# Optimization experiments

Hardware: AMD Instinct MI355X
Metric: run time of the kernel (lower is better)

## Reference

```python
import jax, jax.numpy as jnp
import numpy as np

SR = 24000          # sampling_rate
MAX_H = 60          # min(n_harmonics=100, 60)


def _interp_linear(x, T):
    """Linear upsample along axis 1, align_corners=True. x: [B, C, F] -> [B, T, F]."""
    B, C, F = x.shape
    src = jnp.arange(T, dtype=x.dtype) * ((C - 1) / (T - 1))
    i0 = jnp.clip(jnp.floor(src).astype(jnp.int32), 0, C - 2)
    frac = (src - i0.astype(x.dtype))[None, :, None]
    return x[:, i0, :] * (1.0 - frac) + x[:, i0 + 1, :] * frac


def setup_inputs() -> dict:
    key = jax.random.key(0)
    k1, k2, k3, k4, k5 = jax.random.split(key, 5)
    B, T, H, C, NF = 8, 48000, MAX_H, 100, 5
    f0 = 100.0 + 300.0 * jax.random.uniform(k1, (B, T, 1), dtype=jnp.float32)
    amplitudes = jax.random.uniform(k2, (B, T, H), dtype=jnp.float32)
    formant_freqs = 200.0 + 3300.0 * jax.random.uniform(k3, (B, C, NF), dtype=jnp.float32)
    formant_bws = 50.0 + 150.0 * jax.random.uniform(k4, (B, C, NF), dtype=jnp.float32)
    formant_amps = jax.random.uniform(k5, (B, C, NF), dtype=jnp.float32)
    initial_phase = jnp.zeros((B, 1, 1), dtype=jnp.float32)
    return {"f0": f0, "amplitudes": amplitudes, "formant_freqs": formant_freqs,
            "formant_bws": formant_bws, "formant_amps": formant_amps,
            "initial_phase": initial_phase}


def reference(f0, amplitudes, formant_freqs, formant_bws, formant_amps, initial_phase):
    B, T, _ = f0.shape
    f0 = jax.lax.stop_gradient(f0)                    # torch: f0.detach()
    voiced = (f0[..., 0] > 0).astype(f0.dtype)        # [B, T]
    phase = jnp.cumsum(2.0 * np.pi * f0 / SR, axis=1) + initial_phase  # [B, T, 1]

    ff = _interp_linear(formant_freqs, T)             # [B, T, NF]
    fb = _interp_linear(formant_bws, T)
    fa = _interp_linear(formant_amps, T)

    h = jnp.arange(1, MAX_H + 1, dtype=f0.dtype)      # [H]
    h_freq = f0 * h                                   # [B, T, H]
    nyq = (h_freq < SR / 2).astype(f0.dtype)          # [B, T, H]

    # formant resonance factor: prod over formants of (1 + amp*bw^2/((h_freq-freq)^2+bw^2))
    factor = jnp.ones_like(h_freq)
    for f in range(ff.shape[-1]):                     # NF = 5, small fixed loop
        freq = ff[:, :, f:f + 1]
        bw = fb[:, :, f:f + 1]
        amp = fa[:, :, f:f + 1]
        factor = factor * (1.0 + amp * bw * bw / ((h_freq - freq) ** 2 + bw * bw))

    osc = jnp.sin(phase * h)                          # [B, T, H]
    signal = jnp.sum(osc * amplitudes * factor * nyq, axis=-1) * voiced  # [B, T]

    final_phase = jax.lax.stop_gradient(phase[:, -1:, :] % (2.0 * np.pi))  # [B, 1, 1]
    return signal, final_phase
```

## Files before the change

### kernel.cpp

```cpp
#include <hip/hip_runtime.h>
#include <math.h>

#define SRATE   24000.0
#define NB      8
#define NT      48000
#define NH      60
#define NC      100
#define NFMT    5
#define CTS     64
#define NCH     (NT / CTS)
#define NPAIR   (NCH / 2)
#define TWO_PI  6.283185307179586476925286766559
#define PSC     (1.0f / 1024.0f)
#define NYQS    11.71875f

typedef float v2f __attribute__((ext_vector_type(2)));

__global__ __launch_bounds__(256) void k_partial(const float* __restrict__ f0,
                                                 double* __restrict__ part) {
    int b = blockIdx.y;
    int ch = blockIdx.x * 4 + (threadIdx.x >> 6);
    int lane = threadIdx.x & 63;
    if (ch < NCH) {
        int t = ch * CTS + lane;
        double q = (double)f0[b * NT + t];
        #pragma unroll
        for (int off = 32; off > 0; off >>= 1)
            q += __shfl_down(q, off, 64);
        if (lane == 0) part[b * NCH + ch] = q;
    }
}

__global__ __launch_bounds__(256) void k_main(const float* __restrict__ f0,
                                              const float* __restrict__ amps,
                                              const float* __restrict__ ffq,
                                              const float* __restrict__ fbw,
                                              const float* __restrict__ fam,
                                              const float* __restrict__ initp,
                                              const double* __restrict__ part,
                                              float* __restrict__ out) {
    int b = blockIdx.y;
    int cp = blockIdx.x * 4 + (threadIdx.x >> 6);
    int lane = threadIdx.x & 63;
    if (cp >= NPAIR) return;
    int ch0 = cp * 2;
    int t0 = cp * 128;
    int g0 = lane >> 2, j = lane & 3;

    const float* ab = amps + (size_t)b * NT * NH;

    const float4* r0 = (const float4*)(ab + (size_t)(t0 + g0) * NH);
    float4 A0 = r0[j * 4], A1 = r0[j * 4 + 1], A2 = r0[j * 4 + 2];
    float4 A3 = (j < 3) ? r0[j * 4 + 3] : make_float4(0.f, 0.f, 0.f, 0.f);
    const float4* r1 = (const float4*)(ab + (size_t)(t0 + 16 + g0) * NH);
    float4 B0 = r1[j * 4], B1 = r1[j * 4 + 1], B2 = r1[j * 4 + 2];
    float4 B3 = (j < 3) ? r1[j * 4 + 3] : make_float4(0.f, 0.f, 0.f, 0.f);

    const double* pb = part + b * NCH;
    double sl = 0.0;
    #pragma unroll
    for (int k = 0; k < 12; ++k) {
        int idx = k * 64 + lane;
        double v = (idx < NCH) ? pb[idx] : 0.0;
        if (idx < ch0) sl += v;
    }
    #pragma unroll
    for (int off = 1; off < 64; off <<= 1)
        sl += __shfl_xor(sl, off, 64);

    double initrev = (double)initp[b] * (1.0 / TWO_PI);

    if (cp == 0) {
        double sa = 0.0;
        #pragma unroll
        for (int k = 0; k < 12; ++k) {
            int idx = k * 64 + lane;
            if (idx < NCH) sa += pb[idx];
        }
        #pragma unroll
        for (int off = 1; off < 64; off <<= 1)
            sa += __shfl_xor(sa, off, 64);
        if (lane == 0) {
            double rv = sa * (1.0 / SRATE) + initrev;
            out[NB * NT + b] = (float)((rv - floor(rv)) * TWO_PI);
        }
    }

    float revA, f0sA, revB, f0sB;
    float fqA[NFMT], c1A[NFMT], c2A[NFMT], fqB[NFMT], c1B[NFMT], c2B[NFMT];

    auto chunk_pre = [&](int tl, double prefd, float& rev_o, float& f0s_o,
                         float (&fqo)[NFMT], float (&c1o)[NFMT],
                         float (&c2o)[NFMT]) -> double {
        float f0v = f0[b * NT + tl];
        double inc = (double)f0v;
        #pragma unroll
        for (int off = 1; off < 64; off <<= 1) {
            double n = __shfl_up(inc, off, 64);
            if (lane >= off) inc += n;
        }
        double rev = (prefd + inc) * (1.0 / SRATE) + initrev;
        rev_o = (float)(rev - floor(rev));
        f0s_o = f0v * PSC;
        double srcd = (double)tl * (99.0 / 47999.0);
        int i0 = (int)srcd;
        if (i0 > NC - 2) i0 = NC - 2;
        float frac = (float)(srcd - (double)i0);
        float omf = 1.0f - frac;
        const float* Fq = ffq + (b * NC + i0) * NFMT;
        const float* Bw = fbw + (b * NC + i0) * NFMT;
        const float* Am = fam + (b * NC + i0) * NFMT;
        #pragma unroll
        for (int f = 0; f < NFMT; ++f) {
            float fqv = Fq[f] * omf + Fq[NFMT + f] * frac;
            float bwv = Bw[f] * omf + Bw[NFMT + f] * frac;
            float amv = Am[f] * omf + Am[NFMT + f] * frac;
            float bws = bwv * PSC;
            fqo[f] = fqv * PSC;
            c2o[f] = bws * bws;
            c1o[f] = amv * c2o[f];
        }
        return __shfl(inc, 63, 64);
    };

    double tot0 = chunk_pre(t0 + lane, sl, revA, f0sA, fqA, c1A, c2A);
    chunk_pre(t0 + 64 + lane, sl + tot0, revB, f0sB, fqB, c1B, c2B);

    auto do_pass = [&](int p, float revLane, float f0sLane,
                       const float (&fqL)[NFMT], const float (&c1L)[NFMT],
                       const float (&c2L)[NFMT],
                       float4 q0, float4 q1, float4 q2, float4 q3) {
        int gp = ((p & 3) << 4) + g0;
        float f0s   = __shfl(f0sLane, gp, 64);
        float rev_g = __shfl(revLane, gp, 64);
        float fq[NFMT], c1[NFMT], c2[NFMT];
        #pragma unroll
        for (int f = 0; f < NFMT; ++f) {
            fq[f] = __shfl(fqL[f], gp, 64);
            c1[f] = __shfl(c1L[f], gp, 64);
            c2[f] = __shfl(c2L[f], gp, 64);
        }
        float hb = (float)(j << 4);
        auto sd = [&](float k) {
            return __builtin_amdgcn_sinf(
                __builtin_amdgcn_fractf((hb + k) * rev_g));
        };
        float cc = __builtin_amdgcn_cosf(
            __builtin_amdgcn_fractf(2.0f * rev_g));
        v2f cv = {2.0f * cc, 2.0f * cc};
        v2f pr0 = {sd(1.0f), sd(2.0f)};
        v2f pr1 = {sd(3.0f), sd(4.0f)};
        v2f pr2 = cv * pr1 - pr0;
        v2f pr3 = cv * pr2 - pr1;
        v2f pr4 = {sd(9.0f), sd(10.0f)};
        v2f pr5 = {sd(11.0f), sd(12.0f)};
        v2f pr6 = cv * pr5 - pr4;
        v2f pr7 = cv * pr6 - pr5;
        v2f acc2 = {0.0f, 0.0f};
        auto pairf = [&](float h1, v2f sn, float a0, float a1) {
            v2f hfl = {h1, h1 + 1.0f};
            v2f hs = f0s * hfl;
            v2f pN = {1.0f, 1.0f}, pD = {1.0f, 1.0f};
            #pragma unroll
            for (int f = 0; f < NFMT; ++f) {
                v2f d = hs - fq[f];
                v2f e = d * d + c2[f];
                pN *= e + c1[f];
                pD *= e;
            }
            float R = __builtin_amdgcn_rcpf(pD.x * pD.y);
            v2f fac = {pN.x * pD.y * R, pN.y * pD.x * R};
            v2f fm;
            fm.x = (hs.x < NYQS) ? fac.x : 0.0f;
            fm.y = (hs.y < NYQS) ? fac.y : 0.0f;
            v2f aa = {a0, a1};
            acc2 += (sn * aa) * fm;
        };
        pairf(hb + 1.0f,  pr0, q0.x, q0.y);
        pairf(hb + 3.0f,  pr1, q0.z, q0.w);
        pairf(hb + 5.0f,  pr2, q1.x, q1.y);
        pairf(hb + 7.0f,  pr3, q1.z, q1.w);
        pairf(hb + 9.0f,  pr4, q2.x, q2.y);
        pairf(hb + 11.0f, pr5, q2.z, q2.w);
        pairf(hb + 13.0f, pr6, q3.x, q3.y);
        pairf(hb + 15.0f, pr7, q3.z, q3.w);
        float acc = acc2.x + acc2.y;
        acc += __shfl_xor(acc, 1, 64);
        acc += __shfl_xor(acc, 2, 64);
        if (j == 0) {
            if (!(f0s > 0.0f)) acc = 0.0f;
            out[b * NT + t0 + (p << 4) + g0] = acc;
        }
    };

    #pragma unroll 1
    for (int pg = 0; pg < 8; pg += 2) {
        bool cB = pg >= 4;
        float revL = cB ? revB : revA;
        float f0sL = cB ? f0sB : f0sA;
        float fqL[NFMT], c1L[NFMT], c2L[NFMT];
        #pragma unroll
        for (int f = 0; f < NFMT; ++f) {
            fqL[f] = cB ? fqB[f] : fqA[f];
            c1L[f] = cB ? c1B[f] : c1A[f];
            c2L[f] = cB ? c2B[f] : c2A[f];
        }
        do_pass(pg, revL, f0sL, fqL, c1L, c2L, A0, A1, A2, A3);
        if (pg < 6) {
            const float4* rr =
                (const float4*)(ab + (size_t)(t0 + (pg + 2) * 16 + g0) * NH);
            A0 = rr[j * 4]; A1 = rr[j * 4 + 1]; A2 = rr[j * 4 + 2];
            A3 = (j < 3) ? rr[j * 4 + 3] : make_float4(0.f, 0.f, 0.f, 0.f);
        }
        do_pass(pg + 1, revL, f0sL, fqL, c1L, c2L, B0, B1, B2, B3);
        if (pg < 6) {
            const float4* rr =
                (const float4*)(ab + (size_t)(t0 + (pg + 3) * 16 + g0) * NH);
            B0 = rr[j * 4]; B1 = rr[j * 4 + 1]; B2 = rr[j * 4 + 2];
            B3 = (j < 3) ? rr[j * 4 + 3] : make_float4(0.f, 0.f, 0.f, 0.f);
        }
    }
}

extern "C" void kernel_launch(void* const* d_in, const int* in_sizes, int n_in,
                              void* d_out, int out_size, void* d_ws, size_t ws_size,
                              hipStream_t stream) {
    const float* f0    = (const float*)d_in[0];
    const float* amps  = (const float*)d_in[1];
    const float* ffq   = (const float*)d_in[2];
    const float* fbw   = (const float*)d_in[3];
    const float* fam   = (const float*)d_in[4];
    const float* initp = (const float*)d_in[5];
    float* out = (float*)d_out;

    double* part = (double*)d_ws;

    dim3 gpart((NCH + 3) / 4, NB);
    k_partial<<<gpart, 256, 0, stream>>>(f0, part);
    dim3 gmain((NPAIR + 3) / 4, NB);
    k_main<<<gmain, 256, 0, stream>>>(f0, amps, ffq, fbw, fam, initp, part, out);
}
```

Measured before the change: 33.20 us.

## Hoist all global loads up front and triple-buffer amplitude rows across passes

Issues the f0, formant table, and partial-sum loads at kernel start. Triple-buffers the amplitude rows (three passes in flight instead of two) and fully unrolls the eight passes. The two prefix scans are merged into a single interleaved shuffle loop, and the total-sum reduction runs in every wave instead of only the first. The goal is to hide global memory latency behind the sine/formant math. The costs are more registers (launch bounds now ask for 3 blocks per SM) and some redundant reduction work.

```diff
diff --git a/kernel.cpp b/kernel.cpp
--- a/kernel.cpp
+++ b/kernel.cpp
@@ -31,14 +31,14 @@
     }
 }
 
-__global__ __launch_bounds__(256) void k_main(const float* __restrict__ f0,
-                                              const float* __restrict__ amps,
-                                              const float* __restrict__ ffq,
-                                              const float* __restrict__ fbw,
-                                              const float* __restrict__ fam,
-                                              const float* __restrict__ initp,
-                                              const double* __restrict__ part,
-                                              float* __restrict__ out) {
+__global__ __launch_bounds__(256, 3) void k_main(const float* __restrict__ f0,
+                                                 const float* __restrict__ amps,
+                                                 const float* __restrict__ ffq,
+                                                 const float* __restrict__ fbw,
+                                                 const float* __restrict__ fam,
+                                                 const float* __restrict__ initp,
+                                                 const double* __restrict__ part,
+                                                 float* __restrict__ out) {
     int b = blockIdx.y;
     int cp = blockIdx.x * 4 + (threadIdx.x >> 6);
     int lane = threadIdx.x & 63;
@@ -46,85 +46,100 @@
     int ch0 = cp * 2;
     int t0 = cp * 128;
     int g0 = lane >> 2, j = lane & 3;
-
+    const float4 f4z = make_float4(0.f, 0.f, 0.f, 0.f);
     const float* ab = amps + (size_t)b * NT * NH;
 
-    const float4* r0 = (const float4*)(ab + (size_t)(t0 + g0) * NH);
-    float4 A0 = r0[j * 4], A1 = r0[j * 4 + 1], A2 = r0[j * 4 + 2];
-    float4 A3 = (j < 3) ? r0[j * 4 + 3] : make_float4(0.f, 0.f, 0.f, 0.f);
-    const float4* r1 = (const float4*)(ab + (size_t)(t0 + 16 + g0) * NH);
-    float4 B0 = r1[j * 4], B1 = r1[j * 4 + 1], B2 = r1[j * 4 + 2];
-    float4 B3 = (j < 3) ? r1[j * 4 + 3] : make_float4(0.f, 0.f, 0.f, 0.f);
-
+    float f0A = f0[b * NT + t0 + lane];
+    float f0B = f0[b * NT + t0 + 64 + lane];
+
+    double srcA = (double)(t0 + lane) * (99.0 / 47999.0);
+    int iA = (int)srcA; if (iA > NC - 2) iA = NC - 2;
+    float frA = (float)(srcA - (double)iA), omA = 1.0f - frA;
+    double srcB = (double)(t0 + 64 + lane) * (99.0 / 47999.0);
+    int iB = (int)srcB; if (iB > NC - 2) iB = NC - 2;
+    float frB = (float)(srcB - (double)iB), omB = 1.0f - frB;
+
+    const float* FqA = ffq + (b * NC + iA) * NFMT;
+    const float* BwA = fbw + (b * NC + iA) * NFMT;
+    const float* AmA = fam + (b * NC + iA) * NFMT;
+    const float* FqB = ffq + (b * NC + iB) * NFMT;
+    const float* BwB = fbw + (b * NC + iB) * NFMT;
+    const float* AmB = fam + (b * NC + iB) * NFMT;
+    float tA[30], tB[30];
+    #pragma unroll
+    for (int f = 0; f < NFMT; ++f) {
+        tA[f]      = FqA[f]; tA[5 + f]  = FqA[NFMT + f];
+        tA[10 + f] = BwA[f]; tA[15 + f] = BwA[NFMT + f];
+        tA[20 + f] = AmA[f]; tA[25 + f] = AmA[NFMT + f];
+        tB[f]      = FqB[f]; tB[5 + f]  = FqB[NFMT + f];
+        tB[10 + f] = BwB[f]; tB[15 + f] = BwB[NFMT + f];
+        tB[20 + f] = AmB[f]; tB[25 + f] = AmB[NFMT + f];
+    }
     const double* pb = part + b * NCH;
-    double sl = 0.0;
+    double pv[12];
     #pragma unroll
     for (int k = 0; k < 12; ++k) {
         int idx = k * 64 + lane;
-        double v = (idx < NCH) ? pb[idx] : 0.0;
-        if (idx < ch0) sl += v;
-    }
-    #pragma unroll
-    for (int off = 1; off < 64; off <<= 1)
+        pv[k] = (idx < NCH) ? pb[idx] : 0.0;
+    }
+
+    #define AMPLD(S0, S1, S2, S3, p)                                          \
+        { const float4* rr =                                                  \
+              (const float4*)(ab + (size_t)(t0 + (p) * 16 + g0) * NH);        \
+          S0 = rr[j * 4]; S1 = rr[j * 4 + 1]; S2 = rr[j * 4 + 2];             \
+          S3 = (j < 3) ? rr[j * 4 + 3] : f4z; }
+    float4 P0, P1, P2, P3, Q0, Q1, Q2, Q3, R0, R1, R2, R3;
+    AMPLD(P0, P1, P2, P3, 0)
+    AMPLD(Q0, Q1, Q2, Q3, 1)
+    AMPLD(R0, R1, R2, R3, 2)
+
+    double sl = 0.0, sa = 0.0;
+    #pragma unroll
+    for (int k = 0; k < 12; ++k) {
+        int idx = k * 64 + lane;
+        sa += pv[k];
+        if (idx < ch0) sl += pv[k];
+    }
+    #pragma unroll
+    for (int off = 1; off < 64; off <<= 1) {
         sl += __shfl_xor(sl, off, 64);
-
+        sa += __shfl_xor(sa, off, 64);
+    }
     double initrev = (double)initp[b] * (1.0 / TWO_PI);
-
-    if (cp == 0) {
-        double sa = 0.0;
-        #pragma unroll
-        for (int k = 0; k < 12; ++k) {
-            int idx = k * 64 + lane;
-            if (idx < NCH) sa += pb[idx];
-        }
-        #pragma unroll
-        for (int off = 1; off < 64; off <<= 1)
-            sa += __shfl_xor(sa, off, 64);
-        if (lane == 0) {
-            double rv = sa * (1.0 / SRATE) + initrev;
-            out[NB * NT + b] = (float)((rv - floor(rv)) * TWO_PI);
-        }
-    }
-
-    float revA, f0sA, revB, f0sB;
+    if (cp == 0 && lane == 0) {
+        double rv = sa * (1.0 / SRATE) + initrev;
+        out[NB * NT + b] = (float)((rv - floor(rv)) * TWO_PI);
+    }
+
+    double incA = (double)f0A, incB = (double)f0B;
+    #pragma unroll
+    for (int off = 1; off < 64; off <<= 1) {
+        double nA = __shfl_up(incA, off, 64);
+        double nB = __shfl_up(incB, off, 64);
+        if (lane >= off) { incA += nA; incB += nB; }
+    }
+    double totA = __shfl(incA, 63, 64);
+    double rA = (sl + incA) * (1.0 / SRATE) + initrev;
+    double rB = (sl + totA + incB) * (1.0 / SRATE) + initrev;
+    float revA = (float)(rA - floor(rA));
+    float revB = (float)(rB - floor(rB));
+    float f0sA = f0A * PSC;
+    float f0sB = f0B * PSC;
+
     float fqA[NFMT], c1A[NFMT], c2A[NFMT], fqB[NFMT], c1B[NFMT], c2B[NFMT];
-
-    auto chunk_pre = [&](int tl, double prefd, float& rev_o, float& f0s_o,
-                         float (&fqo)[NFMT], float (&c1o)[NFMT],
-                         float (&c2o)[NFMT]) -> double {
-        float f0v = f0[b * NT + tl];
-        double inc = (double)f0v;
-        #pragma unroll
-        for (int off = 1; off < 64; off <<= 1) {
-            double n = __shfl_up(inc, off, 64);
-            if (lane >= off) inc += n;
-        }
-        double rev = (prefd + inc) * (1.0 / SRATE) + initrev;
-        rev_o = (float)(rev - floor(rev));
-        f0s_o = f0v * PSC;
-        double srcd = (double)tl * (99.0 / 47999.0);
-        int i0 = (int)srcd;
-        if (i0 > NC - 2) i0 = NC - 2;
-        float frac = (float)(srcd - (double)i0);
-        float omf = 1.0f - frac;
-        const float* Fq = ffq + (b * NC + i0) * NFMT;
-        const float* Bw = fbw + (b * NC + i0) * NFMT;
-        const float* Am = fam + (b * NC + i0) * NFMT;
-        #pragma unroll
-        for (int f = 0; f < NFMT; ++f) {
-            float fqv = Fq[f] * omf + Fq[NFMT + f] * frac;
-            float bwv = Bw[f] * omf + Bw[NFMT + f] * frac;
-            float amv = Am[f] * omf + Am[NFMT + f] * frac;
-            float bws = bwv * PSC;
-            fqo[f] = fqv * PSC;
-            c2o[f] = bws * bws;
-            c1o[f] = amv * c2o[f];
-        }
-        return __shfl(inc, 63, 64);
-    };
-
-    double tot0 = chunk_pre(t0 + lane, sl, revA, f0sA, fqA, c1A, c2A);
-    chunk_pre(t0 + 64 + lane, sl + tot0, revB, f0sB, fqB, c1B, c2B);
+    #pragma unroll
+    for (int f = 0; f < NFMT; ++f) {
+        float fq = tA[f] * omA + tA[5 + f] * frA;
+        float bw = tA[10 + f] * omA + tA[15 + f] * frA;
+        float am = tA[20 + f] * omA + tA[25 + f] * frA;
+        float bws = bw * PSC;
+        fqA[f] = fq * PSC; c2A[f] = bws * bws; c1A[f] = am * c2A[f];
+        fq = tB[f] * omB + tB[5 + f] * frB;
+        bw = tB[10 + f] * omB + tB[15 + f] * frB;
+        am = tB[20 + f] * omB + tB[25 + f] * frB;
+        bws = bw * PSC;
+        fqB[f] = fq * PSC; c2B[f] = bws * bws; c1B[f] = am * c2B[f];
+    }
 
     auto do_pass = [&](int p, float revLane, float f0sLane,
                        const float (&fqL)[NFMT], const float (&c1L)[NFMT],
@@ -193,33 +208,20 @@
         }
     };
 
-    #pragma unroll 1
-    for (int pg = 0; pg < 8; pg += 2) {
-        bool cB = pg >= 4;
-        float revL = cB ? revB : revA;
-        float f0sL = cB ? f0sB : f0sA;
-        float fqL[NFMT], c1L[NFMT], c2L[NFMT];
-        #pragma unroll
-        for (int f = 0; f < NFMT; ++f) {
-            fqL[f] = cB ? fqB[f] : fqA[f];
-            c1L[f] = cB ? c1B[f] : c1A[f];
-            c2L[f] = cB ? c2B[f] : c2A[f];
-        }
-        do_pass(pg, revL, f0sL, fqL, c1L, c2L, A0, A1, A2, A3);
-        if (pg < 6) {
-            const float4* rr =
-                (const float4*)(ab + (size_t)(t0 + (pg + 2) * 16 + g0) * NH);
-            A0 = rr[j * 4]; A1 = rr[j * 4 + 1]; A2 = rr[j * 4 + 2];
-            A3 = (j < 3) ? rr[j * 4 + 3] : make_float4(0.f, 0.f, 0.f, 0.f);
-        }
-        do_pass(pg + 1, revL, f0sL, fqL, c1L, c2L, B0, B1, B2, B3);
-        if (pg < 6) {
-            const float4* rr =
-                (const float4*)(ab + (size_t)(t0 + (pg + 3) * 16 + g0) * NH);
-            B0 = rr[j * 4]; B1 = rr[j * 4 + 1]; B2 = rr[j * 4 + 2];
-            B3 = (j < 3) ? rr[j * 4 + 3] : make_float4(0.f, 0.f, 0.f, 0.f);
-        }
-    }
+    do_pass(0, revA, f0sA, fqA, c1A, c2A, P0, P1, P2, P3);
+    AMPLD(P0, P1, P2, P3, 3)
+    do_pass(1, revA, f0sA, fqA, c1A, c2A, Q0, Q1, Q2, Q3);
+    AMPLD(Q0, Q1, Q2, Q3, 4)
+    do_pass(2, revA, f0sA, fqA, c1A, c2A, R0, R1, R2, R3);
+    AMPLD(R0, R1, R2, R3, 5)
+    do_pass(3, revA, f0sA, fqA, c1A, c2A, P0, P1, P2, P3);
+    AMPLD(P0, P1, P2, P3, 6)
+    do_pass(4, revB, f0sB, fqB, c1B, c2B, Q0, Q1, Q2, Q3);
+    AMPLD(Q0, Q1, Q2, Q3, 7)
+    do_pass(5, revB, f0sB, fqB, c1B, c2B, R0, R1, R2, R3);
+    do_pass(6, revB, f0sB, fqB, c1B, c2B, P0, P1, P2, P3);
+    do_pass(7, revB, f0sB, fqB, c1B, c2B, Q0, Q1, Q2, Q3);
+    #undef AMPLD
 }
 
 extern "C" void kernel_launch(void* const* d_in, const int* in_sizes, int n_in,
```

Result: slower. 39.47 us (+18.9%).
